# Performance work log

Hardware: AMD Instinct MI355X
Metric: run time of the kernel (lower is better)

The kernel has to match this reference:

```python
import jax, jax.numpy as jnp
import numpy as np

N_HEAD = 16
D_MODEL = 1024
HEAD_SIZE = D_MODEL // N_HEAD
BATCH, SEQ = 2, 2048


def setup_inputs() -> dict:
    key = jax.random.key(0)
    ks = jax.random.split(key, 11)
    s = 1.0 / np.sqrt(D_MODEL)
    inp = {
        "query": jax.random.normal(ks[0], (BATCH, SEQ, D_MODEL), jnp.float32),
        "key_in": jax.random.normal(ks[1], (BATCH, SEQ, D_MODEL), jnp.float32),
        "value": jax.random.normal(ks[2], (BATCH, SEQ, D_MODEL), jnp.float32),
        # per-head Q/K/V projections stacked: [n_head, d_model, head_size]
        "Wq": jax.random.uniform(ks[3], (N_HEAD, D_MODEL, HEAD_SIZE), jnp.float32, -s, s),
        "Wk": jax.random.uniform(ks[4], (N_HEAD, D_MODEL, HEAD_SIZE), jnp.float32, -s, s),
        "Wv": jax.random.uniform(ks[5], (N_HEAD, D_MODEL, HEAD_SIZE), jnp.float32, -s, s),
        "bq": jax.random.uniform(ks[6], (N_HEAD, HEAD_SIZE), jnp.float32, -s, s),
        "bk": jax.random.uniform(ks[7], (N_HEAD, HEAD_SIZE), jnp.float32, -s, s),
        "bv": jax.random.uniform(ks[8], (N_HEAD, HEAD_SIZE), jnp.float32, -s, s),
        "Wo": jax.random.uniform(ks[9], (D_MODEL, D_MODEL), jnp.float32, -s, s),
        "bo": jax.random.uniform(ks[10], (D_MODEL,), jnp.float32, -s, s),
    }
    return inp


def reference(query, key_in, value, Wq, Wk, Wv, bq, bk, bv, Wo, bo):
    # Per-head projections fused into one einsum each: [b, h, s, k]
    Q = jnp.einsum("bsd,hdk->bhsk", query, Wq) + bq[:, None, :]
    K = jnp.einsum("bsd,hdk->bhsk", key_in, Wk) + bk[:, None, :]
    V = jnp.einsum("bsd,hdk->bhsk", value, Wv) + bv[:, None, :]
    scale = 1.0 / np.sqrt(HEAD_SIZE)
    wei = jnp.einsum("bhqk,bhsk->bhqs", Q, K) * scale  # [b, h, s, s]
    wei = jax.nn.softmax(wei, axis=-1)
    out = jnp.einsum("bhqs,bhsk->bhqk", wei, V)  # [b, h, s, k]
    b, h, s, k = out.shape
    out = out.transpose(0, 2, 1, 3).reshape(b, s, h * k)
    return out @ Wo.T + bo
```

## Files before the change

kernel.cpp:

```cpp
#include <hip/hip_runtime.h>
#include <hip/hip_bf16.h>

typedef __attribute__((ext_vector_type(8))) short short8;
typedef __attribute__((ext_vector_type(4))) short bf16x4;
typedef __attribute__((ext_vector_type(4))) float f32x4;

#define DM 1024
#define NH 16
#define HS 64
#define SEQL 2048

__device__ __forceinline__ float bf2f(short s) {
  unsigned u = ((unsigned)(unsigned short)s) << 16;
  float f;
  __builtin_memcpy(&f, &u, 4);
  return f;
}
__device__ __forceinline__ short f2bf(float f) {
  unsigned u;
  __builtin_memcpy(&u, &f, 4);
  u = u + 0x7FFFu + ((u >> 16) & 1u);
  return (short)(u >> 16);
}

__global__ __launch_bounds__(256) void pack_w_kernel(
    const float* __restrict__ Wq, const float* __restrict__ Wk, const float* __restrict__ Wv,
    short* __restrict__ WtQ, short* __restrict__ WtK, short* __restrict__ WtV) {
  const float* W = (blockIdx.z == 0) ? Wq : (blockIdx.z == 1) ? Wk : Wv;
  short* Wt      = (blockIdx.z == 0) ? WtQ : (blockIdx.z == 1) ? WtK : WtV;
  __shared__ short Ts[64][73];
  const int h = blockIdx.y, dm0 = blockIdx.x * 64;
  const int tid = threadIdx.x;
#pragma unroll
  for (int p = 0; p < 4; ++p) {
    int idx = p * 256 + tid;
    int i = idx >> 4, hsq = (idx & 15) * 4;
    f32x4 v = *(const f32x4*)&W[((h << 10) + dm0 + i) * 64 + hsq];
#pragma unroll
    for (int j = 0; j < 4; ++j) Ts[i][hsq + j] = f2bf(v[j]);
  }
  __syncthreads();
  {
    int hs = tid >> 2, dmq = (tid & 3) * 16;
    short8 o0, o1;
#pragma unroll
    for (int j = 0; j < 8; ++j) { o0[j] = Ts[dmq + j][hs]; o1[j] = Ts[dmq + 8 + j][hs]; }
    short* dst = &Wt[((h * 64 + hs) << 10) + dm0 + dmq];
    *(short8*)dst = o0;
    *(short8*)(dst + 8) = o1;
  }
}

struct GemmArgs {
  const void* A;
  const void* Bt;
  const float* bias;
  short* out;
  float* outf;
  int mode;
};

template <bool AFP32, bool BFP32>
__global__ __launch_bounds__(256) void gemm_bt_kernel(GemmArgs g0, GemmArgs g1, GemmArgs g2) {
  GemmArgs g = (blockIdx.z == 0) ? g0 : (blockIdx.z == 1) ? g1 : g2;
  const int K = 1024;
  const int m0 = blockIdx.x * 128;
  const int n0 = blockIdx.y * 128;
  const int tid = threadIdx.x;
  const int w = tid >> 6, l = tid & 63, lr = l & 15, lk = l >> 4;
  const int wr = w >> 1, wc = w & 1;

  __shared__ __align__(16) short As[128][40];
  __shared__ __align__(16) short Bs[128][40];

  f32x4 acc[4][4];
#pragma unroll
  for (int i = 0; i < 4; ++i)
#pragma unroll
    for (int j = 0; j < 4; ++j) acc[i][j] = (f32x4){0.f, 0.f, 0.f, 0.f};

  for (int k0 = 0; k0 < K; k0 += 32) {
    __syncthreads();
#pragma unroll
    for (int i = 0; i < 2; ++i) {
      int q = tid * 2 + i;
      int row = q >> 2, kc = (q & 3) * 8;
      short8 av, bv;
      if (AFP32) {
        const f32x4* ap = (const f32x4*)((const float*)g.A + (size_t)(m0 + row) * K + k0 + kc);
        f32x4 f0 = ap[0], f1 = ap[1];
#pragma unroll
        for (int j = 0; j < 4; ++j) { av[j] = f2bf(f0[j]); av[4 + j] = f2bf(f1[j]); }
      } else {
        av = *(const short8*)((const short*)g.A + (size_t)(m0 + row) * K + k0 + kc);
      }
      if (BFP32) {
        const f32x4* bp = (const f32x4*)((const float*)g.Bt + (size_t)(n0 + row) * K + k0 + kc);
        f32x4 f0 = bp[0], f1 = bp[1];
#pragma unroll
        for (int j = 0; j < 4; ++j) { bv[j] = f2bf(f0[j]); bv[4 + j] = f2bf(f1[j]); }
      } else {
        bv = *(const short8*)((const short*)g.Bt + (size_t)(n0 + row) * K + k0 + kc);
      }
      *(short8*)&As[row][kc] = av;
      *(short8*)&Bs[row][kc] = bv;
    }
    __syncthreads();
    short8 af[4], bfr[4];
#pragma unroll
    for (int t = 0; t < 4; ++t) {
      af[t]  = *(const short8*)&As[wr * 64 + t * 16 + lr][lk * 8];
      bfr[t] = *(const short8*)&Bs[wc * 64 + t * 16 + lr][lk * 8];
    }
#pragma unroll
    for (int ti = 0; ti < 4; ++ti)
#pragma unroll
      for (int tj = 0; tj < 4; ++tj)
        acc[ti][tj] = __builtin_amdgcn_mfma_f32_16x16x32_bf16(af[ti], bfr[tj], acc[ti][tj], 0, 0, 0);
  }

#pragma unroll
  for (int ti = 0; ti < 4; ++ti)
#pragma unroll
    for (int tj = 0; tj < 4; ++tj) {
      int n = n0 + wc * 64 + tj * 16 + lr;
      float bia = g.bias[n];
      int mb = m0 + wr * 64 + ti * 16 + lk * 4;
      if (g.mode == 2) {
        bf16x4 o;
#pragma unroll
        for (int r = 0; r < 4; ++r) o[r] = f2bf(acc[ti][tj][r] + bia);
        *(bf16x4*)&g.out[((mb >> 11) * 16 + (n >> 6)) * (SEQL * HS) + (n & 63) * SEQL + (mb & 2047)] = o;
      } else {
#pragma unroll
        for (int r = 0; r < 4; ++r) {
          int m = mb + r;
          float v = acc[ti][tj][r] + bia;
          if (g.mode == 0) {
            g.out[((m >> 11) * 16 + (n >> 6)) * (SEQL * HS) + (m & 2047) * HS + (n & 63)] = f2bf(v);
          } else {
            g.outf[(size_t)m * DM + n] = v;
          }
        }
      }
    }
}

__global__ __launch_bounds__(256, 4) void attn_kernel(const short* __restrict__ Qg, const short* __restrict__ Kg,
                                                      const short* __restrict__ Vtg, short* __restrict__ Og) {
  const int qt = blockIdx.x;
  const int bh = blockIdx.y;
  const short* Qp = Qg + bh * SEQL * HS;
  const short* Kp = Kg + bh * SEQL * HS;
  const short* Vp = Vtg + bh * HS * SEQL;
  const int tid = threadIdx.x, w = tid >> 6, l = tid & 63, lr = l & 15, lk = l >> 4;
  const int qw = qt * 64 + w * 16;

  __shared__ __align__(16) short Ks[128][72];
  __shared__ __align__(16) short Vt[64][136];

  short8 qf[2];
#pragma unroll
  for (int kk = 0; kk < 2; ++kk) {
    short8 qr = *(const short8*)&Qp[(qw + lr) * HS + kk * 32 + lk * 8];
#pragma unroll
    for (int j = 0; j < 8; ++j) qf[kk][j] = f2bf(bf2f(qr[j]) * 0.125f);
  }

  float mrow = -1e30f, lrow = 0.f;
  f32x4 accO[4];
#pragma unroll
  for (int t = 0; t < 4; ++t) accO[t] = (f32x4){0.f, 0.f, 0.f, 0.f};

  for (int kv = 0; kv < 16; ++kv) {
    __syncthreads();
#pragma unroll
    for (int i = 0; i < 4; ++i) {
      int q = tid + i * 256;
      int row = q >> 3, col = (q & 7) * 8;
      *(short8*)&Ks[row][col] = *(const short8*)&Kp[(kv * 128 + row) * HS + col];
    }
#pragma unroll
    for (int i = 0; i < 4; ++i) {
      int q = tid + i * 256;
      int d = q >> 4, sc = (q & 15) * 8;
      *(short8*)&Vt[d][sc] = *(const short8*)&Vp[d * SEQL + kv * 128 + sc];
    }
    __syncthreads();

    f32x4 accS[8];
#pragma unroll
    for (int tj = 0; tj < 8; ++tj) {
      short8 a0 = *(const short8*)&Ks[tj * 16 + lr][lk * 8];
      short8 a1 = *(const short8*)&Ks[tj * 16 + lr][32 + lk * 8];
      f32x4 z = (f32x4){0.f, 0.f, 0.f, 0.f};
      z = __builtin_amdgcn_mfma_f32_16x16x32_bf16(a0, qf[0], z, 0, 0, 0);
      accS[tj] = __builtin_amdgcn_mfma_f32_16x16x32_bf16(a1, qf[1], z, 0, 0, 0);
    }

    float mx = accS[0][0];
#pragma unroll
    for (int tj = 0; tj < 8; ++tj)
#pragma unroll
      for (int r = 0; r < 4; ++r) mx = fmaxf(mx, accS[tj][r]);
    mx = fmaxf(mx, __shfl_xor(mx, 16));
    mx = fmaxf(mx, __shfl_xor(mx, 32));
    float mn = fmaxf(mrow, mx);
    float alpha = __expf(mrow - mn);
    float ps = 0.f;
#pragma unroll
    for (int tj = 0; tj < 8; ++tj)
#pragma unroll
      for (int r = 0; r < 4; ++r) {
        float p = __expf(accS[tj][r] - mn);
        accS[tj][r] = p;
        ps += p;
      }
    ps += __shfl_xor(ps, 16);
    ps += __shfl_xor(ps, 32);
    lrow = lrow * alpha + ps;
    mrow = mn;
#pragma unroll
    for (int t = 0; t < 4; ++t) accO[t] *= alpha;

#pragma unroll
    for (int st = 0; st < 8; ++st) {
      bf16x4 bfrag;
#pragma unroll
      for (int r = 0; r < 4; ++r) bfrag[r] = f2bf(accS[st][r]);
#pragma unroll
      for (int tjd = 0; tjd < 4; ++tjd) {
        bf16x4 afrag = *(const bf16x4*)&Vt[tjd * 16 + lr][st * 16 + lk * 4];
        accO[tjd] = __builtin_amdgcn_mfma_f32_16x16x16bf16_1k(afrag, bfrag, accO[tjd], 0, 0, 0);
      }
    }
  }

  const int b = bh >> 4, h = bh & 15;
  float inv = 1.f / lrow;
  size_t rowbase = (size_t)(b * SEQL + qw + lr) * DM + h * HS;
#pragma unroll
  for (int tjd = 0; tjd < 4; ++tjd) {
    bf16x4 o;
#pragma unroll
    for (int r = 0; r < 4; ++r) o[r] = f2bf(accO[tjd][r] * inv);
    *(bf16x4*)&Og[rowbase + tjd * 16 + lk * 4] = o;
  }
}

extern "C" void kernel_launch(void* const* d_in, const int* in_sizes, int n_in,
                              void* d_out, int out_size, void* d_ws, size_t ws_size,
                              hipStream_t stream) {
  const float* query  = (const float*)d_in[0];
  const float* key_in = (const float*)d_in[1];
  const float* value  = (const float*)d_in[2];
  const float* Wq = (const float*)d_in[3];
  const float* Wk = (const float*)d_in[4];
  const float* Wv = (const float*)d_in[5];
  const float* bq = (const float*)d_in[6];
  const float* bk = (const float*)d_in[7];
  const float* bv = (const float*)d_in[8];
  const float* Wo = (const float*)d_in[9];
  const float* bo = (const float*)d_in[10];
  float* out = (float*)d_out;

  short* ws  = (short*)d_ws;
  short* Qb  = ws;
  short* Kb  = Qb + (4 << 20);
  short* Vbt = Kb + (4 << 20);
  short* X   = Vbt + (4 << 20);
  short* WtQ = X;
  short* WtK = WtQ + (1 << 20);
  short* WtV = WtK + (1 << 20);
  short* At  = X;

  pack_w_kernel<<<dim3(16, 16, 3), 256, 0, stream>>>(Wq, Wk, Wv, WtQ, WtK, WtV);

  GemmArgs gq{query, WtQ, bq, Qb, nullptr, 0}, gk{key_in, WtK, bk, Kb, nullptr, 0},
           gv{value, WtV, bv, Vbt, nullptr, 2};
  gemm_bt_kernel<true, false><<<dim3(32, 8, 3), 256, 0, stream>>>(gq, gk, gv);

  attn_kernel<<<dim3(32, 32), 256, 0, stream>>>(Qb, Kb, Vbt, At);

  GemmArgs go{At, Wo, bo, nullptr, out, 1};
  gemm_bt_kernel<false, true><<<dim3(32, 8, 1), 256, 0, stream>>>(go, go, go);
}
```

Measured before the change: 323.8 us.

## Use direct global-to-LDS loads with swizzled tiles in projection GEMMs

The GEMM kernel now stages A and B tiles with global_load_lds (direct global-to-LDS DMA) into XOR-swizzled, unpadded shared arrays instead of loading through registers. For fp32 A inputs, fp32 is staged in LDS and converted with packed v_cvt_pk_bf16_f32 at fragment load time. Wo is pre-converted to bf16 by a separate kernel, and the output GEMM uses a narrower N tile (64) to double its block count. This removes register round-trips and per-element conversion in the load loop, at the cost of an extra launch, a Wo conversion pass and more LDS for fp32 A tiles.

After: 289.9 us. -10.5%, faster.

```diff
diff --git a/kernel.cpp b/kernel.cpp
--- a/kernel.cpp
+++ b/kernel.cpp
@@ -21,6 +21,21 @@
   __builtin_memcpy(&u, &f, 4);
   u = u + 0x7FFFu + ((u >> 16) & 1u);
   return (short)(u >> 16);
+}
+
+__device__ __forceinline__ void gl2lds16(const void* g, void* l) {
+  __builtin_amdgcn_global_load_lds(
+      (const __attribute__((address_space(1))) void*)g,
+      (__attribute__((address_space(3))) void*)l, 16, 0, 0);
+}
+
+__device__ __forceinline__ short8 cvt_pk8(f32x4 lo, f32x4 hi) {
+  union { short8 s8; unsigned u[4]; } r;
+  asm("v_cvt_pk_bf16_f32 %0, %1, %2" : "=v"(r.u[0]) : "v"(lo[0]), "v"(lo[1]));
+  asm("v_cvt_pk_bf16_f32 %0, %1, %2" : "=v"(r.u[1]) : "v"(lo[2]), "v"(lo[3]));
+  asm("v_cvt_pk_bf16_f32 %0, %1, %2" : "=v"(r.u[2]) : "v"(hi[0]), "v"(hi[1]));
+  asm("v_cvt_pk_bf16_f32 %0, %1, %2" : "=v"(r.u[3]) : "v"(hi[2]), "v"(hi[3]));
+  return r.s8;
 }
 
 __global__ __launch_bounds__(256) void pack_w_kernel(
@@ -51,6 +66,17 @@
   }
 }
 
+__global__ __launch_bounds__(256) void cvt_bf16_kernel(const float* __restrict__ in,
+                                                       short* __restrict__ out) {
+  int i = blockIdx.x * 256 + threadIdx.x;
+  const f32x4* p = (const f32x4*)(in + (size_t)i * 8);
+  f32x4 a = p[0], b = p[1];
+  short8 o;
+#pragma unroll
+  for (int j = 0; j < 4; ++j) { o[j] = f2bf(a[j]); o[4 + j] = f2bf(b[j]); }
+  *(short8*)(out + (size_t)i * 8) = o;
+}
+
 struct GemmArgs {
   const void* A;
   const void* Bt;
@@ -60,70 +86,94 @@
   int mode;
 };
 
-template <bool AFP32, bool BFP32>
+template <bool AF32, int NB>
 __global__ __launch_bounds__(256) void gemm_bt_kernel(GemmArgs g0, GemmArgs g1, GemmArgs g2) {
   GemmArgs g = (blockIdx.z == 0) ? g0 : (blockIdx.z == 1) ? g1 : g2;
   const int K = 1024;
+  const int TN = NB * 32;
   const int m0 = blockIdx.x * 128;
-  const int n0 = blockIdx.y * 128;
+  const int n0 = blockIdx.y * TN;
   const int tid = threadIdx.x;
   const int w = tid >> 6, l = tid & 63, lr = l & 15, lk = l >> 4;
   const int wr = w >> 1, wc = w & 1;
 
-  __shared__ __align__(16) short As[128][40];
-  __shared__ __align__(16) short Bs[128][40];
-
-  f32x4 acc[4][4];
+  __shared__ __align__(16) char AsRaw[128 * 32 * (AF32 ? 4 : 2)];
+  __shared__ __align__(16) short Bs[TN * 32];
+  float* Asf = (float*)AsRaw;
+  short* As  = (short*)AsRaw;
+
+  const int swz3 = lr & 7;
+  const int swz2 = (lr & 3) ^ ((lr >> 2) & 3);
+
+  f32x4 acc[4][NB];
 #pragma unroll
   for (int i = 0; i < 4; ++i)
 #pragma unroll
-    for (int j = 0; j < 4; ++j) acc[i][j] = (f32x4){0.f, 0.f, 0.f, 0.f};
+    for (int j = 0; j < NB; ++j) acc[i][j] = (f32x4){0.f, 0.f, 0.f, 0.f};
 
   for (int k0 = 0; k0 < K; k0 += 32) {
     __syncthreads();
-#pragma unroll
-    for (int i = 0; i < 2; ++i) {
-      int q = tid * 2 + i;
-      int row = q >> 2, kc = (q & 3) * 8;
-      short8 av, bv;
-      if (AFP32) {
-        const f32x4* ap = (const f32x4*)((const float*)g.A + (size_t)(m0 + row) * K + k0 + kc);
-        f32x4 f0 = ap[0], f1 = ap[1];
-#pragma unroll
-        for (int j = 0; j < 4; ++j) { av[j] = f2bf(f0[j]); av[4 + j] = f2bf(f1[j]); }
+    if constexpr (AF32) {
+      const float* Af = (const float*)g.A;
+#pragma unroll
+      for (int i = 0; i < 4; ++i) {
+        int c = i * 256 + tid;
+        int row = c >> 3, s = c & 7;
+        int gc = (s ^ (row & 7)) * 4;
+        gl2lds16(&Af[(size_t)(m0 + row) * K + k0 + gc], &Asf[c * 4]);
+      }
+    } else {
+      const short* Ah = (const short*)g.A;
+#pragma unroll
+      for (int i = 0; i < 2; ++i) {
+        int c = i * 256 + tid;
+        int row = c >> 2, s = c & 3;
+        int gc = (s ^ ((row & 3) ^ ((row >> 2) & 3))) * 8;
+        gl2lds16(&Ah[(size_t)(m0 + row) * K + k0 + gc], &As[c * 8]);
+      }
+    }
+    {
+      const short* Bh = (const short*)g.Bt;
+#pragma unroll
+      for (int i = 0; i < TN / 64; ++i) {
+        int c = i * 256 + tid;
+        int row = c >> 2, s = c & 3;
+        int gc = (s ^ ((row & 3) ^ ((row >> 2) & 3))) * 8;
+        gl2lds16(&Bh[(size_t)(n0 + row) * K + k0 + gc], &Bs[c * 8]);
+      }
+    }
+    __syncthreads();
+
+    short8 af[4], bfr[NB];
+#pragma unroll
+    for (int t = 0; t < 4; ++t) {
+      int row = wr * 64 + t * 16 + lr;
+      if constexpr (AF32) {
+        int base = row * 32;
+        f32x4 lo = *(const f32x4*)&Asf[base + (((lk << 1)    ) ^ swz3) * 4];
+        f32x4 hi = *(const f32x4*)&Asf[base + (((lk << 1) | 1) ^ swz3) * 4];
+        af[t] = cvt_pk8(lo, hi);
       } else {
-        av = *(const short8*)((const short*)g.A + (size_t)(m0 + row) * K + k0 + kc);
-      }
-      if (BFP32) {
-        const f32x4* bp = (const f32x4*)((const float*)g.Bt + (size_t)(n0 + row) * K + k0 + kc);
-        f32x4 f0 = bp[0], f1 = bp[1];
-#pragma unroll
-        for (int j = 0; j < 4; ++j) { bv[j] = f2bf(f0[j]); bv[4 + j] = f2bf(f1[j]); }
-      } else {
-        bv = *(const short8*)((const short*)g.Bt + (size_t)(n0 + row) * K + k0 + kc);
-      }
-      *(short8*)&As[row][kc] = av;
-      *(short8*)&Bs[row][kc] = bv;
-    }
-    __syncthreads();
-    short8 af[4], bfr[4];
-#pragma unroll
-    for (int t = 0; t < 4; ++t) {
-      af[t]  = *(const short8*)&As[wr * 64 + t * 16 + lr][lk * 8];
-      bfr[t] = *(const short8*)&Bs[wc * 64 + t * 16 + lr][lk * 8];
+        af[t] = *(const short8*)&As[row * 32 + (lk ^ swz2) * 8];
+      }
+    }
+#pragma unroll
+    for (int t = 0; t < NB; ++t) {
+      int row = wc * (NB * 16) + t * 16 + lr;
+      bfr[t] = *(const short8*)&Bs[row * 32 + (lk ^ swz2) * 8];
     }
 #pragma unroll
     for (int ti = 0; ti < 4; ++ti)
 #pragma unroll
-      for (int tj = 0; tj < 4; ++tj)
+      for (int tj = 0; tj < NB; ++tj)
         acc[ti][tj] = __builtin_amdgcn_mfma_f32_16x16x32_bf16(af[ti], bfr[tj], acc[ti][tj], 0, 0, 0);
   }
 
 #pragma unroll
   for (int ti = 0; ti < 4; ++ti)
 #pragma unroll
-    for (int tj = 0; tj < 4; ++tj) {
-      int n = n0 + wc * 64 + tj * 16 + lr;
+    for (int tj = 0; tj < NB; ++tj) {
+      int n = n0 + wc * (NB * 16) + tj * 16 + lr;
       float bia = g.bias[n];
       int mb = m0 + wr * 64 + ti * 16 + lk * 4;
       if (g.mode == 2) {
@@ -273,15 +323,18 @@
   short* WtK = WtQ + (1 << 20);
   short* WtV = WtK + (1 << 20);
   short* At  = X;
+  short* Wob = Qb;
 
   pack_w_kernel<<<dim3(16, 16, 3), 256, 0, stream>>>(Wq, Wk, Wv, WtQ, WtK, WtV);
 
   GemmArgs gq{query, WtQ, bq, Qb, nullptr, 0}, gk{key_in, WtK, bk, Kb, nullptr, 0},
            gv{value, WtV, bv, Vbt, nullptr, 2};
-  gemm_bt_kernel<true, false><<<dim3(32, 8, 3), 256, 0, stream>>>(gq, gk, gv);
+  gemm_bt_kernel<true, 4><<<dim3(32, 8, 3), 256, 0, stream>>>(gq, gk, gv);
 
   attn_kernel<<<dim3(32, 32), 256, 0, stream>>>(Qb, Kb, Vbt, At);
 
-  GemmArgs go{At, Wo, bo, nullptr, out, 1};
-  gemm_bt_kernel<false, true><<<dim3(32, 8, 1), 256, 0, stream>>>(go, go, go);
-}
+  cvt_bf16_kernel<<<dim3(512), 256, 0, stream>>>(Wo, Wob);
+
+  GemmArgs go{At, Wob, bo, nullptr, out, 1};
+  gemm_bt_kernel<false, 2><<<dim3(32, 16, 1), 256, 0, stream>>>(go, go, go);
+}
```
